# Kernel tuning notes

Hardware: AMD Instinct MI355X
Metric: run time of the kernel (lower is better)

Reference implementation:

```python
import jax, jax.numpy as jnp
import numpy as np

B, W, T, D = 8, 64, 256, 256
TI, WL, WP, G = 32, 16, 24, 64


def _ln(x, g, b):
    mu = jnp.mean(x, -1, keepdims=True)
    v = jnp.mean((x - mu) ** 2, -1, keepdims=True)
    return (x - mu) * jax.lax.rsqrt(v + 1e-5) * g + b


def _mlp2(x, w1, b1, w2, b2):
    return jax.nn.relu(x @ w1 + b1) @ w2 + b2


def setup_inputs():
    key = jax.random.key(0)
    ks = jax.random.split(key, 48)
    it = iter(range(48))
    def n(shape, s=0.02):
        return jax.random.normal(ks[next(it)], shape, jnp.float32) * s
    return {
        "task_obs": n((B, T, TI), 1.0),
        "worker_loads": n((B, W, WL), 1.0),
        "worker_profiles": n((B, W, WP), 1.0),
        "global_context": n((B, G), 1.0),
        "valid_mask": jax.random.randint(ks[next(it)], (B, T), 0, 2).astype(jnp.float32),
        "te_w1": n((TI, D)), "te_b1": jnp.zeros((D,)), "te_w2": n((D, D)), "te_b2": jnp.zeros((D,)),
        "wle_w1": n((WL, D)), "wle_b1": jnp.zeros((D,)), "wle_w2": n((D, D)), "wle_b2": jnp.zeros((D,)),
        "wpe_w1": n((WP, D)), "wpe_b1": jnp.zeros((D,)), "wpe_w2": n((D, D)), "wpe_b2": jnp.zeros((D,)),
        "ft_w": n((D, D)), "ft_b": jnp.zeros((D,)), "ft_g": jnp.ones((D,)), "ft_bt": jnp.zeros((D,)),
        "fw_w": n((2 * D, D)), "fw_b": jnp.zeros((D,)), "fw_g": jnp.ones((D,)), "fw_bt": jnp.zeros((D,)),
        "g_w1": n((G, D)), "g_b1": jnp.zeros((D,)), "g_w2": n((D, D)), "g_b2": jnp.zeros((D,)),
        "fn_g": jnp.ones((3 * D,)), "fn_b": jnp.zeros((3 * D,)),
        "actor_w": n((3 * D, 1)), "actor_b": jnp.zeros((1,)),
        "log_std": jnp.zeros((W, T)),
        "vu_w1": n((3 * D, D)), "vu_b1": jnp.zeros((D,)), "vu_w2": n((D, 1)), "vu_b2": jnp.zeros((1,)),
        "vc_w1": n((3 * D, D)), "vc_b1": jnp.zeros((D,)), "vc_w2": n((D, 1)), "vc_b2": jnp.zeros((1,)),
        "policy_id": 2,
    }


def reference(task_obs, worker_loads, worker_profiles, global_context, valid_mask, te_w1, te_b1, te_w2, te_b2, wle_w1, wle_b1, wle_w2, wle_b2, wpe_w1, wpe_b1, wpe_w2, wpe_b2, ft_w, ft_b, ft_g, ft_bt, fw_w, fw_b, fw_g, fw_bt, g_w1, g_b1, g_w2, g_b2, fn_g, fn_b, actor_w, actor_b, log_std, vu_w1, vu_b1, vu_w2, vu_b2, vc_w1, vc_b1, vc_w2, vc_b2, policy_id):
    b = task_obs.shape[0]
    # encoders (RowWiseEncoder = 2-layer MLP) + per-modality projections
    t_feat = _ln(jax.nn.relu(_mlp2(task_obs, te_w1, te_b1, te_w2, te_b2) @ ft_w + ft_b), ft_g, ft_bt)  # (B,T,D)
    wl = _mlp2(worker_loads, wle_w1, wle_b1, wle_w2, wle_b2)
    wp = _mlp2(worker_profiles, wpe_w1, wpe_b1, wpe_w2, wpe_b2)
    w_feat = _ln(jax.nn.relu(jnp.concatenate([wl, wp], -1) @ fw_w + fw_b), fw_g, fw_bt)  # (B,W,D)
    g_feat = jax.nn.relu(global_context @ g_w1 + g_b1) @ g_w2 + g_b2  # (B,D)
    # broadcast + concat fusion (B,W,T,3D), LayerNorm, actor head
    w_exp = jnp.broadcast_to(w_feat[:, :, None, :], (b, W, T, D))
    t_exp = jnp.broadcast_to(t_feat[:, None, :, :], (b, W, T, D))
    g_exp = jnp.broadcast_to(g_feat[:, None, None, :], (b, W, T, D))
    fusion = _ln(jnp.concatenate([w_exp, t_exp, g_exp], -1), fn_g, fn_b)
    mean = jax.nn.sigmoid((fusion @ actor_w)[..., 0] + actor_b[0])  # (B,W,T)
    std = jnp.broadcast_to(jnp.exp(jnp.clip(log_std, -4.0, 1.0))[None], mean.shape)
    # masked mean pooling + value heads
    mask = valid_mask[..., None]
    t_pool = (t_feat * mask).sum(1) / jnp.clip(mask.sum(1), 1.0, None)
    w_pool = w_feat.mean(1)
    vci = jnp.concatenate([t_pool, w_pool, g_feat], -1)  # (B,3D)
    v_u = _mlp2(vci, vu_w1, vu_b1, vu_w2, vu_b2)[..., 0]
    v_c = _mlp2(vci, vc_w1, vc_b1, vc_w2, vc_b2)[..., 0]
    return (mean, std, v_u, v_c)
```

## Files before the change

kernel.cpp:

```cpp
#include <hip/hip_runtime.h>
#include <math.h>

namespace {

constexpr int B_ = 8, W_ = 64, T_ = 256, D_ = 256;

typedef _Float16 h2 __attribute__((ext_vector_type(2)));
typedef _Float16 h8 __attribute__((ext_vector_type(8)));
typedef float f32x4 __attribute__((ext_vector_type(4)));
typedef __fp16 fp16v2 __attribute__((ext_vector_type(2)));

constexpr int WS_ST    = 0;
constexpr int WS_SUMT  = 2048;
constexpr int WS_SST   = 4096;
constexpr int WS_SW    = 6144;
constexpr int WS_SUMW  = 6656;
constexpr int WS_SSW   = 7168;
constexpr int WS_SG    = 7680;
constexpr int WS_SUMG  = 7688;
constexpr int WS_SSG   = 7696;
constexpr int WS_C0    = 7704;
constexpr int WS_C1    = 7705;
constexpr int WS_GFEAT = 7712;
constexpr int WS_TPP   = 9760;
constexpr int WS_WPP   = 42528;
constexpr int WS_PK    = 665120;

constexpr int FM_TE1  = 0;
constexpr int FM_TE2  = 1024;
constexpr int FM_FT   = 9216;
constexpr int FM_WLE1 = 17408;
constexpr int FM_WLE2 = 18432;
constexpr int FM_WPE1 = 26624;
constexpr int FM_WPE2 = 27648;
constexpr int FM_FW   = 35840;
constexpr int FM_END  = 52224;
constexpr int PM_G1   = 52224;
constexpr int PM_G2   = 54272;
constexpr int PM_VU1  = 62464;
constexpr int PM_VC1  = 87040;
constexpr int PK_TOTAL = 111616;

__device__ __forceinline__ float wave_sum(float v) {
#pragma unroll
  for (int m = 32; m > 0; m >>= 1) v += __shfl_xor(v, m, 64);
  return v;
}

__device__ __forceinline__ float red16(float v) {
  v += __shfl_xor(v, 1, 64);
  v += __shfl_xor(v, 2, 64);
  v += __shfl_xor(v, 4, 64);
  v += __shfl_xor(v, 8, 64);
  return v;
}

__device__ __forceinline__ unsigned pkrtz_u(float a, float b) {
  fp16v2 p = __builtin_amdgcn_cvt_pkrtz(a, b);
  return __builtin_bit_cast(unsigned, p);
}

__device__ __forceinline__ float fdot2u(unsigned x, unsigned w, float c) {
#if __has_builtin(__builtin_amdgcn_fdot2)
  return __builtin_amdgcn_fdot2(__builtin_bit_cast(h2, x),
                                __builtin_bit_cast(h2, w), c, false);
#else
  h2 a = __builtin_bit_cast(h2, x);
  h2 b = __builtin_bit_cast(h2, w);
  float r = fmaf((float)a.x, (float)b.x, c);
  return fmaf((float)a.y, (float)b.y, r);
#endif
}

template <int R, int G>
__device__ __forceinline__ void gemmp(const uint4* __restrict__ Wp,
                                      const uint4* xp, int xs, int d,
                                      float* acc) {
#pragma unroll
  for (int r = 0; r < R; ++r) acc[r] = 0.f;
#pragma unroll 4
  for (int g = 0; g < G; ++g) {
    uint4 w = Wp[g * 256 + d];
#pragma unroll
    for (int r = 0; r < R; ++r) {
      uint4 x = xp[r * xs + g];
      acc[r] = fdot2u(x.x, w.x, acc[r]);
      acc[r] = fdot2u(x.y, w.y, acc[r]);
      acc[r] = fdot2u(x.z, w.z, acc[r]);
      acc[r] = fdot2u(x.w, w.w, acc[r]);
    }
  }
}

template <int R>
__device__ __forceinline__ void shfl_pack(const float* v, unsigned* dst,
                                          int stride, int d) {
#pragma unroll
  for (int r = 0; r < R; ++r) {
    float p = __shfl_xor(v[r], 1, 64);
    unsigned pk = (d & 1) ? pkrtz_u(p, v[r]) : pkrtz_u(v[r], p);
    if (!(d & 1)) dst[r * stride + (d >> 1)] = pk;
  }
}

template <int NT, int KS, bool ACC_IN>
__device__ __forceinline__ void mfma_gemm(const uint4* __restrict__ wb,
                                          int nt0, int ks0, int l,
                                          const h8* afr, f32x4* acc) {
  uint4 bufA[KS], bufB[KS];
#pragma unroll
  for (int ks = 0; ks < KS; ++ks)
    bufA[ks] = wb[((ks0 + ks) * 16 + nt0) * 64 + l];
#pragma unroll
  for (int nt = 0; nt < NT; ++nt) {
    const uint4* cur = (nt & 1) ? bufB : bufA;
    uint4* nxt = (nt & 1) ? bufA : bufB;
    if (nt + 1 < NT) {
#pragma unroll
      for (int ks = 0; ks < KS; ++ks)
        nxt[ks] = wb[((ks0 + ks) * 16 + nt0 + nt + 1) * 64 + l];
    }
    f32x4 c;
    if (ACC_IN) c = acc[nt];
    else { c[0] = 0.f; c[1] = 0.f; c[2] = 0.f; c[3] = 0.f; }
#pragma unroll
    for (int ks = 0; ks < KS; ++ks)
      c = __builtin_amdgcn_mfma_f32_16x16x32_f16(
          afr[ks], __builtin_bit_cast(h8, cur[ks]), c, 0, 0, 0);
    acc[nt] = c;
  }
}

template <int KS>
__device__ __forceinline__ void lda(const _Float16* src, int row, int stride,
                                    int l4, h8* afr) {
#pragma unroll
  for (int ks = 0; ks < KS; ++ks)
    afr[ks] = *(const h8*)(src + row * stride + ks * 32 + 8 * l4);
}

template <int NT, bool RELU>
__device__ __forceinline__ void epi_store(const f32x4* acc,
                                          const float* __restrict__ bias,
                                          int c0, int dc0, int l15, int l4,
                                          _Float16* dst, int stride) {
#pragma unroll
  for (int nt = 0; nt < NT; ++nt) {
    float bv = bias[c0 + nt * 16 + l15];
    int dc = dc0 + nt * 16 + l15;
#pragma unroll
    for (int i = 0; i < 4; ++i) {
      float v = acc[nt][i] + bv;
      if (RELU) v = fmaxf(v, 0.f);
      dst[(l4 * 4 + i) * stride + dc] = (_Float16)v;
    }
  }
}

template <bool MASKED>
__device__ __forceinline__ void ln_block8(
    f32x4* acc, const float* __restrict__ g, const float* __restrict__ bt,
    const float* __restrict__ fn_g_seg, const float* __restrict__ aw_seg,
    const float* __restrict__ mask_base, float* stA, float* stB, int wq, int l,
    int tid, float* __restrict__ pool, float* __restrict__ Sd,
    float* __restrict__ sumd, float* __restrict__ ssd) {
  const int l15 = l & 15, l4 = l >> 4;
#pragma unroll
  for (int i = 0; i < 4; ++i) {
    float s = 0.f, ss = 0.f;
#pragma unroll
    for (int nt = 0; nt < 2; ++nt) {
      float v = acc[nt][i];
      s += v;
      ss = fmaf(v, v, ss);
    }
    s = red16(s);
    ss = red16(ss);
    if (l15 == 0) {
      int row = l4 * 4 + i;
      stA[(row * 8 + wq) * 2 + 0] = s;
      stA[(row * 8 + wq) * 2 + 1] = ss;
    }
  }
  __syncthreads();
  float gg[2], bb[2], fa[2];
#pragma unroll
  for (int nt = 0; nt < 2; ++nt) {
    int c = wq * 32 + nt * 16 + l15;
    gg[nt] = g[c];
    bb[nt] = bt[c];
    fa[nt] = fn_g_seg[c] * aw_seg[c];
  }
  float pp[2] = {0.f, 0.f};
#pragma unroll
  for (int i = 0; i < 4; ++i) {
    int row = l4 * 4 + i;
    float s = 0.f, ss = 0.f;
#pragma unroll
    for (int q = 0; q < 8; ++q) {
      s += stA[(row * 8 + q) * 2];
      ss += stA[(row * 8 + q) * 2 + 1];
    }
    float mu = s * (1.f / 256.f);
    float var = ss * (1.f / 256.f) - mu * mu;
    float inv = rsqrtf(var + 1e-5f);
    float mk = MASKED ? mask_base[row] : 1.f;
    float a1 = 0.f, a2 = 0.f, a3 = 0.f;
#pragma unroll
    for (int nt = 0; nt < 2; ++nt) {
      float v = (acc[nt][i] - mu) * inv * gg[nt] + bb[nt];
      a1 = fmaf(v, fa[nt], a1);
      a2 += v;
      a3 = fmaf(v, v, a3);
      pp[nt] = fmaf(mk, v, pp[nt]);
    }
    a1 = red16(a1);
    a2 = red16(a2);
    a3 = red16(a3);
    if (l15 == 0) {
      stB[(row * 8 + wq) * 3 + 0] = a1;
      stB[(row * 8 + wq) * 3 + 1] = a2;
      stB[(row * 8 + wq) * 3 + 2] = a3;
    }
  }
#pragma unroll
  for (int nt = 0; nt < 2; ++nt) {
    pp[nt] += __shfl_xor(pp[nt], 16, 64);
    pp[nt] += __shfl_xor(pp[nt], 32, 64);
  }
  if (l < 16) {
#pragma unroll
    for (int nt = 0; nt < 2; ++nt) pool[wq * 32 + nt * 16 + l15] = pp[nt];
  }
  __syncthreads();
  if (tid < 16) {
    int row = tid;
    float sA = 0.f, sB = 0.f, sC = 0.f;
#pragma unroll
    for (int q = 0; q < 8; ++q) {
      sA += stB[(row * 8 + q) * 3 + 0];
      sB += stB[(row * 8 + q) * 3 + 1];
      sC += stB[(row * 8 + q) * 3 + 2];
    }
    Sd[row] = sA;
    sumd[row] = sB;
    ssd[row] = sC;
  }
}

__global__ __launch_bounds__(256) void pack_kernel(
    const float* __restrict__ te_w1, const float* __restrict__ te_w2,
    const float* __restrict__ ft_w, const float* __restrict__ wle_w1,
    const float* __restrict__ wle_w2, const float* __restrict__ wpe_w1,
    const float* __restrict__ wpe_w2, const float* __restrict__ fw_w,
    const float* __restrict__ g_w1, const float* __restrict__ g_w2,
    const float* __restrict__ vu_w1, const float* __restrict__ vc_w1,
    uint4* __restrict__ dst) {
  int i = blockIdx.x * 256 + threadIdx.x;
  if (i < FM_END) {
    const float* src; int off, Ksrc;
    if      (i < FM_TE2)  { src = te_w1;  off = FM_TE1;  Ksrc = 32;  }
    else if (i < FM_FT)   { src = te_w2;  off = FM_TE2;  Ksrc = 256; }
    else if (i < FM_WLE1) { src = ft_w;   off = FM_FT;   Ksrc = 256; }
    else if (i < FM_WLE2) { src = wle_w1; off = FM_WLE1; Ksrc = 16;  }
    else if (i < FM_WPE1) { src = wle_w2; off = FM_WLE2; Ksrc = 256; }
    else if (i < FM_WPE2) { src = wpe_w1; off = FM_WPE1; Ksrc = 24;  }
    else if (i < FM_FW)   { src = wpe_w2; off = FM_WPE2; Ksrc = 256; }
    else                  { src = fw_w;   off = FM_FW;   Ksrc = 512; }
    int li = i - off;
    int l = li & 63, nt = (li >> 6) & 15, ks = li >> 10;
    int n = nt * 16 + (l & 15);
    int k0 = ks * 32 + 8 * (l >> 4);
    h8 v;
#pragma unroll
    for (int j = 0; j < 8; ++j) {
      int k = k0 + j;
      v[j] = (k < Ksrc) ? (_Float16)src[(size_t)k * 256 + n] : (_Float16)0.f;
    }
    dst[i] = __builtin_bit_cast(uint4, v);
  } else {
    const float* src; int off;
    if      (i < PM_G2)  { src = g_w1;  off = PM_G1;  }
    else if (i < PM_VU1) { src = g_w2;  off = PM_G2;  }
    else if (i < PM_VC1) { src = vu_w1; off = PM_VU1; }
    else                 { src = vc_w1; off = PM_VC1; }
    int li = i - off;
    int g = li >> 8, d = li & 255;
    const float* p = src + (size_t)g * 8 * 256 + d;
    unsigned r[4];
#pragma unroll
    for (int j = 0; j < 4; ++j) {
      h2 pk;
      pk.x = (_Float16)p[(2 * j) * 256];
      pk.y = (_Float16)p[(2 * j + 1) * 256];
      r[j] = __builtin_bit_cast(unsigned, pk);
    }
    uint4 o;
    o.x = r[0]; o.y = r[1]; o.z = r[2]; o.w = r[3];
    dst[i] = o;
  }
}

__global__ __launch_bounds__(512) void enc_kernel(
    const float* __restrict__ task_obs, const float* __restrict__ worker_loads,
    const float* __restrict__ worker_profiles,
    const float* __restrict__ global_context,
    const float* __restrict__ valid_mask, const float* __restrict__ te_b1,
    const float* __restrict__ te_b2, const float* __restrict__ wle_b1,
    const float* __restrict__ wle_b2, const float* __restrict__ wpe_b1,
    const float* __restrict__ wpe_b2, const float* __restrict__ ft_b,
    const float* __restrict__ ft_g, const float* __restrict__ ft_bt,
    const float* __restrict__ fw_b, const float* __restrict__ fw_g,
    const float* __restrict__ fw_bt, const float* __restrict__ g_b1,
    const float* __restrict__ g_b2, const float* __restrict__ fn_g,
    const float* __restrict__ fn_b, const float* __restrict__ actor_w,
    const float* __restrict__ actor_b, const uint4* __restrict__ wpk,
    float* __restrict__ ws) {
  __shared__ __align__(16) unsigned char smem[29440];
  const int tid = threadIdx.x;
  const int blk = blockIdx.x;
  const int w = tid >> 6, l = tid & 63;
  const int l15 = l & 15, l4 = l >> 4;
  const int swz = ((blk >> 3) + blk) & 7;
  const int wq = (w + swz) & 7;
  float* stA = (float*)(smem + 26880);
  float* stB = (float*)(smem + 27904);

  if (blk < 128) {
    const int rb = blk * 16;
    const int bI = rb >> 8, t0 = rb & 255;
    _Float16* hT = (_Float16*)smem;
    h8 a0;
    {
      const float* xr = task_obs + (size_t)(rb + l15) * 32 + 8 * l4;
      float4 xa = *(const float4*)xr;
      float4 xb = *(const float4*)(xr + 4);
      a0[0] = (_Float16)xa.x; a0[1] = (_Float16)xa.y;
      a0[2] = (_Float16)xa.z; a0[3] = (_Float16)xa.w;
      a0[4] = (_Float16)xb.x; a0[5] = (_Float16)xb.y;
      a0[6] = (_Float16)xb.z; a0[7] = (_Float16)xb.w;
    }
    f32x4 acc[2];
    mfma_gemm<2, 1, false>(wpk + FM_TE1, 2 * wq, 0, l, &a0, acc);
    epi_store<2, true>(acc, te_b1, wq * 32, wq * 32, l15, l4, hT, 264);
    __syncthreads();
    h8 afr[8];
    lda<8>(hT, l15, 264, l4, afr);
    __syncthreads();
    mfma_gemm<2, 8, false>(wpk + FM_TE2, 2 * wq, 0, l, afr, acc);
    epi_store<2, false>(acc, te_b2, wq * 32, wq * 32, l15, l4, hT, 264);
    __syncthreads();
    lda<8>(hT, l15, 264, l4, afr);
    mfma_gemm<2, 8, false>(wpk + FM_FT, 2 * wq, 0, l, afr, acc);
#pragma unroll
    for (int nt = 0; nt < 2; ++nt) {
      float bv = ft_b[wq * 32 + nt * 16 + l15];
#pragma unroll
      for (int i = 0; i < 4; ++i) acc[nt][i] = fmaxf(acc[nt][i] + bv, 0.f);
    }
    ln_block8<true>(acc, ft_g, ft_bt, fn_g + 256, actor_w + 256,
                    valid_mask + bI * 256 + t0, stA, stB, wq, l, tid,
                    ws + WS_TPP + blk * 256, ws + WS_ST + rb, ws + WS_SUMT + rb,
                    ws + WS_SST + rb);
  } else if (blk < 160) {
    const int wbl = blk - 128;
    const int rbw = wbl * 16;
    _Float16* XW = (_Float16*)smem;
    _Float16* h1 = (_Float16*)(smem + 1536);
    _Float16* ct = (_Float16*)(smem + 9984);
    if (tid < 256) {
      int r = tid >> 4, k = tid & 15;
      XW[r * 48 + k] = (_Float16)worker_loads[(size_t)(rbw + r) * 16 + k];
      XW[r * 48 + 16 + k] = (_Float16)0.f;
    }
    __syncthreads();
    h8 ax = *(const h8*)(XW + l15 * 48 + 8 * l4);
    f32x4 acc[2];
    mfma_gemm<2, 1, false>(wpk + FM_WLE1, 2 * wq, 0, l, &ax, acc);
    epi_store<2, true>(acc, wle_b1, wq * 32, wq * 32, l15, l4, h1, 264);
    __syncthreads();
    h8 afr[8];
    lda<8>(h1, l15, 264, l4, afr);
    for (int e = tid; e < 384; e += 512) {
      int r = e / 24, k = e - r * 24;
      XW[r * 48 + k] = (_Float16)worker_profiles[(size_t)(rbw + r) * 24 + k];
    }
    if (tid < 128) {
      int r = tid >> 3, k = 24 + (tid & 7);
      XW[r * 48 + k] = (_Float16)0.f;
    }
    __syncthreads();
    mfma_gemm<2, 8, false>(wpk + FM_WLE2, 2 * wq, 0, l, afr, acc);
    epi_store<2, false>(acc, wle_b2, wq * 32, wq * 32, l15, l4, ct, 528);
    ax = *(const h8*)(XW + l15 * 48 + 8 * l4);
    mfma_gemm<2, 1, false>(wpk + FM_WPE1, 2 * wq, 0, l, &ax, acc);
    epi_store<2, true>(acc, wpe_b1, wq * 32, wq * 32, l15, l4, h1, 264);
    __syncthreads();
    lda<8>(h1, l15, 264, l4, afr);
    mfma_gemm<2, 8, false>(wpk + FM_WPE2, 2 * wq, 0, l, afr, acc);
    epi_store<2, false>(acc, wpe_b2, wq * 32, 256 + wq * 32, l15, l4, ct, 528);
    __syncthreads();
    h8 af2[16];
    lda<16>(ct, l15, 528, l4, af2);
    mfma_gemm<2, 8, false>(wpk + FM_FW, 2 * wq, 0, l, af2, acc);
    mfma_gemm<2, 8, true>(wpk + FM_FW, 2 * wq, 8, l, af2 + 8, acc);
#pragma unroll
    for (int nt = 0; nt < 2; ++nt) {
      float bv = fw_b[wq * 32 + nt * 16 + l15];
#pragma unroll
      for (int i = 0; i < 4; ++i) acc[nt][i] = fmaxf(acc[nt][i] + bv, 0.f);
    }
    ln_block8<false>(acc, fw_g, fw_bt, fn_g, actor_w, nullptr, stA, stB, wq, l,
                     tid, ws + WS_WPP + wbl * 256, ws + WS_SW + rbw,
                     ws + WS_SUMW + rbw, ws + WS_SSW + rbw);
  } else {
    float* smf = (float*)smem;
    unsigned* smp = (unsigned*)(smem + 8256);
    const int d = tid & 255;
    if (tid < 256)
      smp[tid] = pkrtz_u(global_context[2 * tid], global_context[2 * tid + 1]);
    __syncthreads();
    float acc[8], v[8];
    if (tid < 256) {
      gemmp<8, 8>(wpk + PM_G1, (const uint4*)smp, 8, d, acc);
      float b = g_b1[d];
#pragma unroll
      for (int r = 0; r < 8; ++r) v[r] = fmaxf(acc[r] + b, 0.f);
      shfl_pack<8>(v, smp + 256, 128, d);
    }
    __syncthreads();
    if (tid < 256) {
      gemmp<8, 32>(wpk + PM_G2, (const uint4*)(smp + 256), 32, d, acc);
      float b = g_b2[d];
#pragma unroll
      for (int r = 0; r < 8; ++r) {
        float x = acc[r] + b;
        ws[WS_GFEAT + r * D_ + d] = x;
        smf[r * D_ + d] = x;
      }
      float c0 = 0.f, c1 = 0.f;
      for (int i = tid; i < 768; i += 256) {
        float aw = actor_w[i];
        c0 = fmaf(fn_b[i], aw, c0);
        c1 = fmaf(fn_g[i], aw, c1);
      }
      c0 = wave_sum(c0);
      c1 = wave_sum(c1);
      const int wv = tid >> 6, lane = tid & 63;
      if (lane == 0) {
        smf[2048 + wv] = c0;
        smf[2052 + wv] = c1;
      }
    }
    __syncthreads();
    if (tid < 256) {
      const int wv = tid >> 6, lane = tid & 63;
      for (int r = wv; r < 8; r += 4) {
        float a1 = 0.f, a2 = 0.f, a3 = 0.f;
        for (int j = lane; j < D_; j += 64) {
          float x = smf[r * D_ + j];
          a1 = fmaf(x, fn_g[512 + j] * actor_w[512 + j], a1);
          a2 += x;
          a3 = fmaf(x, x, a3);
        }
        a1 = wave_sum(a1);
        a2 = wave_sum(a2);
        a3 = wave_sum(a3);
        if (lane == 0) {
          ws[WS_SG + r] = a1;
          ws[WS_SUMG + r] = a2;
          ws[WS_SSG + r] = a3;
        }
      }
      if (tid == 0) {
        ws[WS_C0] = smf[2048] + smf[2049] + smf[2050] + smf[2051] + actor_b[0];
        ws[WS_C1] = smf[2052] + smf[2053] + smf[2054] + smf[2055];
      }
    }
  }
}

__global__ __launch_bounds__(256) void head_kernel(
    const float* __restrict__ valid_mask, const float* __restrict__ log_std,
    const float* __restrict__ vu_b1, const float* __restrict__ vu_b2,
    const float* __restrict__ vc_b1, const float* __restrict__ vc_b2,
    const float* __restrict__ vu_w2, const float* __restrict__ vc_w2,
    const uint4* __restrict__ wpk, const float* __restrict__ ws,
    float* __restrict__ out) {
  const int tid = threadIdx.x;
  const int blk = blockIdx.x;
  if (blk < 16) {
    const int head = blk >> 3;
    const int b = blk & 7;
    __shared__ float lm[256];
    __shared__ float red[8];
    __shared__ __align__(16) unsigned vcip[384];
    lm[tid] = valid_mask[b * T_ + tid];
    __syncthreads();
    float m = wave_sum(lm[tid]);
    if ((tid & 63) == 0) red[tid >> 6] = m;
    __syncthreads();
    const float mdiv = 1.f / fmaxf(red[0] + red[1] + red[2] + red[3], 1.f);
    float vv[3];
    {
      float acc = 0.f;
#pragma unroll
      for (int c = 0; c < 16; ++c)
        acc += ws[WS_TPP + (b * 16 + c) * 256 + tid];
      vv[0] = acc * mdiv;
      acc = 0.f;
#pragma unroll
      for (int c = 0; c < 4; ++c) acc += ws[WS_WPP + (b * 4 + c) * 256 + tid];
      vv[1] = acc * (1.f / 64.f);
      vv[2] = ws[WS_GFEAT + b * D_ + tid];
    }
    shfl_pack<3>(vv, vcip, 128, tid);
    __syncthreads();
    const uint4* w1p = wpk + (head ? PM_VC1 : PM_VU1);
    const float* b1 = head ? vc_b1 : vu_b1;
    const float* w2 = head ? vc_w2 : vu_w2;
    const float* b2 = head ? vc_b2 : vu_b2;
    float h = 0.f;
    const uint4* xq = (const uint4*)vcip;
    int g = (blk & 7) * 12;
#pragma unroll 8
    for (int it = 0; it < 96; ++it) {
      uint4 w = w1p[g * 256 + tid];
      uint4 x = xq[g];
      h = fdot2u(x.x, w.x, h);
      h = fdot2u(x.y, w.y, h);
      h = fdot2u(x.z, w.z, h);
      h = fdot2u(x.w, w.w, h);
      ++g;
      if (g == 96) g = 0;
    }
    h = fmaxf(h + b1[tid], 0.f);
    float c = wave_sum(h * w2[tid]);
    __syncthreads();
    if ((tid & 63) == 0) red[tid >> 6] = c;
    __syncthreads();
    if (tid == 0)
      out[2 * B_ * W_ * T_ + head * B_ + b] =
          red[0] + red[1] + red[2] + red[3] + b2[0];
  } else {
    const int base = (blk - 16) * 512 + tid * 2;
    const float C0 = ws[WS_C0];
    const float C1 = ws[WS_C1];
#pragma unroll
    for (int e = 0; e < 2; ++e) {
      const int idx = base + e;
      const int b = idx >> 14;
      const int w = (idx >> 8) & 63;
      const int t = idx & 255;
      float S = ws[WS_SW + b * W_ + w] + ws[WS_ST + b * T_ + t] + ws[WS_SG + b];
      float sum =
          ws[WS_SUMW + b * W_ + w] + ws[WS_SUMT + b * T_ + t] + ws[WS_SUMG + b];
      float ssq =
          ws[WS_SSW + b * W_ + w] + ws[WS_SST + b * T_ + t] + ws[WS_SSG + b];
      float mu = sum * (1.f / 768.f);
      float var = ssq * (1.f / 768.f) - mu * mu;
      float inv = rsqrtf(var + 1e-5f);
      float logit = inv * (S - mu * C1) + C0;
      out[idx] = 1.f / (1.f + expf(-logit));
      float ls = log_std[w * T_ + t];
      out[B_ * W_ * T_ + idx] = expf(fminf(fmaxf(ls, -4.f), 1.f));
    }
  }
}

}

extern "C" void kernel_launch(void* const* d_in, const int* in_sizes, int n_in,
                              void* d_out, int out_size, void* d_ws,
                              size_t ws_size, hipStream_t stream) {
  (void)in_sizes; (void)n_in; (void)out_size; (void)ws_size;
  const float* task_obs        = (const float*)d_in[0];
  const float* worker_loads    = (const float*)d_in[1];
  const float* worker_profiles = (const float*)d_in[2];
  const float* global_context  = (const float*)d_in[3];
  const float* valid_mask      = (const float*)d_in[4];
  const float* te_w1  = (const float*)d_in[5];
  const float* te_b1  = (const float*)d_in[6];
  const float* te_w2  = (const float*)d_in[7];
  const float* te_b2  = (const float*)d_in[8];
  const float* wle_w1 = (const float*)d_in[9];
  const float* wle_b1 = (const float*)d_in[10];
  const float* wle_w2 = (const float*)d_in[11];
  const float* wle_b2 = (const float*)d_in[12];
  const float* wpe_w1 = (const float*)d_in[13];
  const float* wpe_b1 = (const float*)d_in[14];
  const float* wpe_w2 = (const float*)d_in[15];
  const float* wpe_b2 = (const float*)d_in[16];
  const float* ft_w   = (const float*)d_in[17];
  const float* ft_b   = (const float*)d_in[18];
  const float* ft_g   = (const float*)d_in[19];
  const float* ft_bt  = (const float*)d_in[20];
  const float* fw_w   = (const float*)d_in[21];
  const float* fw_b   = (const float*)d_in[22];
  const float* fw_g   = (const float*)d_in[23];
  const float* fw_bt  = (const float*)d_in[24];
  const float* g_w1   = (const float*)d_in[25];
  const float* g_b1   = (const float*)d_in[26];
  const float* g_w2   = (const float*)d_in[27];
  const float* g_b2   = (const float*)d_in[28];
  const float* fn_g   = (const float*)d_in[29];
  const float* fn_b   = (const float*)d_in[30];
  const float* actor_w = (const float*)d_in[31];
  const float* actor_b = (const float*)d_in[32];
  const float* log_std = (const float*)d_in[33];
  const float* vu_w1  = (const float*)d_in[34];
  const float* vu_b1  = (const float*)d_in[35];
  const float* vu_w2  = (const float*)d_in[36];
  const float* vu_b2  = (const float*)d_in[37];
  const float* vc_w1  = (const float*)d_in[38];
  const float* vc_b1  = (const float*)d_in[39];
  const float* vc_w2  = (const float*)d_in[40];
  const float* vc_b2  = (const float*)d_in[41];
  float* ws = (float*)d_ws;
  uint4* wpk = (uint4*)(ws + WS_PK);
  float* out = (float*)d_out;

  hipLaunchKernelGGL(pack_kernel, dim3(PK_TOTAL / 256), dim3(256), 0, stream,
                     te_w1, te_w2, ft_w, wle_w1, wle_w2, wpe_w1, wpe_w2, fw_w,
                     g_w1, g_w2, vu_w1, vc_w1, wpk);
  hipLaunchKernelGGL(enc_kernel, dim3(161), dim3(512), 0, stream, task_obs,
                     worker_loads, worker_profiles, global_context, valid_mask,
                     te_b1, te_b2, wle_b1, wle_b2, wpe_b1, wpe_b2, ft_b, ft_g,
                     ft_bt, fw_b, fw_g, fw_bt, g_b1, g_b2, fn_g, fn_b, actor_w,
                     actor_b, (const uint4*)wpk, ws);
  hipLaunchKernelGGL(head_kernel, dim3(272), dim3(256), 0, stream, valid_mask,
                     log_std, vu_b1, vu_b2, vc_b1, vc_b2, vu_w2, vc_w2,
                     (const uint4*)wpk, (const float*)ws, out);
}
```

Measured before the change: 34.62 us.

## Prefetch next-stage MFMA weight fragments into registers ahead of dependent GEMMs

Weight B-fragments for each subsequent GEMM stage are now loaded into registers before the preceding stage's epilogue and barriers, instead of being fetched right before each GEMM. Global-memory latency for the weights can then overlap with shared-memory staging, syncs and earlier MFMA work in both the task and worker encoder branches. The cost is more live vector registers (up to 48 uint4 fragments held at once), which may lower occupancy or cause spills.

```diff
diff --git a/kernel.cpp b/kernel.cpp
--- a/kernel.cpp
+++ b/kernel.cpp
@@ -103,32 +103,40 @@
   }
 }
 
+template <int NT, int KS>
+__device__ __forceinline__ void load_bfrags(const uint4* __restrict__ wb,
+                                            int nt0, int ks0, int l,
+                                            uint4* pf) {
+#pragma unroll
+  for (int nt = 0; nt < NT; ++nt)
+#pragma unroll
+    for (int ks = 0; ks < KS; ++ks)
+      pf[nt * KS + ks] = wb[((ks0 + ks) * 16 + nt0 + nt) * 64 + l];
+}
+
+template <int NT, int KS, bool ACC_IN>
+__device__ __forceinline__ void mfma_from(const uint4* pf, const h8* afr,
+                                          f32x4* acc) {
+#pragma unroll
+  for (int nt = 0; nt < NT; ++nt) {
+    f32x4 c;
+    if (ACC_IN) c = acc[nt];
+    else { c[0] = 0.f; c[1] = 0.f; c[2] = 0.f; c[3] = 0.f; }
+#pragma unroll
+    for (int ks = 0; ks < KS; ++ks)
+      c = __builtin_amdgcn_mfma_f32_16x16x32_f16(
+          afr[ks], __builtin_bit_cast(h8, pf[nt * KS + ks]), c, 0, 0, 0);
+    acc[nt] = c;
+  }
+}
+
 template <int NT, int KS, bool ACC_IN>
 __device__ __forceinline__ void mfma_gemm(const uint4* __restrict__ wb,
                                           int nt0, int ks0, int l,
                                           const h8* afr, f32x4* acc) {
-  uint4 bufA[KS], bufB[KS];
-#pragma unroll
-  for (int ks = 0; ks < KS; ++ks)
-    bufA[ks] = wb[((ks0 + ks) * 16 + nt0) * 64 + l];
-#pragma unroll
-  for (int nt = 0; nt < NT; ++nt) {
-    const uint4* cur = (nt & 1) ? bufB : bufA;
-    uint4* nxt = (nt & 1) ? bufA : bufB;
-    if (nt + 1 < NT) {
-#pragma unroll
-      for (int ks = 0; ks < KS; ++ks)
-        nxt[ks] = wb[((ks0 + ks) * 16 + nt0 + nt + 1) * 64 + l];
-    }
-    f32x4 c;
-    if (ACC_IN) c = acc[nt];
-    else { c[0] = 0.f; c[1] = 0.f; c[2] = 0.f; c[3] = 0.f; }
-#pragma unroll
-    for (int ks = 0; ks < KS; ++ks)
-      c = __builtin_amdgcn_mfma_f32_16x16x32_f16(
-          afr[ks], __builtin_bit_cast(h8, cur[ks]), c, 0, 0, 0);
-    acc[nt] = c;
-  }
+  uint4 pf[NT * KS];
+  load_bfrags<NT, KS>(wb, nt0, ks0, l, pf);
+  mfma_from<NT, KS, ACC_IN>(pf, afr, acc);
 }
 
 template <int KS>
@@ -330,6 +338,8 @@
     const int rb = blk * 16;
     const int bI = rb >> 8, t0 = rb & 255;
     _Float16* hT = (_Float16*)smem;
+    uint4 pfA[16];
+    load_bfrags<2, 8>(wpk + FM_TE2, 2 * wq, 0, l, pfA);
     h8 a0;
     {
       const float* xr = task_obs + (size_t)(rb + l15) * 32 + 8 * l4;
@@ -347,11 +357,13 @@
     h8 afr[8];
     lda<8>(hT, l15, 264, l4, afr);
     __syncthreads();
-    mfma_gemm<2, 8, false>(wpk + FM_TE2, 2 * wq, 0, l, afr, acc);
+    uint4 pfB[16];
+    load_bfrags<2, 8>(wpk + FM_FT, 2 * wq, 0, l, pfB);
+    mfma_from<2, 8, false>(pfA, afr, acc);
     epi_store<2, false>(acc, te_b2, wq * 32, wq * 32, l15, l4, hT, 264);
     __syncthreads();
     lda<8>(hT, l15, 264, l4, afr);
-    mfma_gemm<2, 8, false>(wpk + FM_FT, 2 * wq, 0, l, afr, acc);
+    mfma_from<2, 8, false>(pfB, afr, acc);
 #pragma unroll
     for (int nt = 0; nt < 2; ++nt) {
       float bv = ft_b[wq * 32 + nt * 16 + l15];
@@ -368,6 +380,8 @@
     _Float16* XW = (_Float16*)smem;
     _Float16* h1 = (_Float16*)(smem + 1536);
     _Float16* ct = (_Float16*)(smem + 9984);
+    uint4 pfA[16];
+    load_bfrags<2, 8>(wpk + FM_WLE2, 2 * wq, 0, l, pfA);
     if (tid < 256) {
       int r = tid >> 4, k = tid & 15;
       XW[r * 48 + k] = (_Float16)worker_loads[(size_t)(rbw + r) * 16 + k];
@@ -381,6 +395,8 @@
     __syncthreads();
     h8 afr[8];
     lda<8>(h1, l15, 264, l4, afr);
+    uint4 pfB[16];
+    load_bfrags<2, 8>(wpk + FM_WPE2, 2 * wq, 0, l, pfB);
     for (int e = tid; e < 384; e += 512) {
       int r = e / 24, k = e - r * 24;
       XW[r * 48 + k] = (_Float16)worker_profiles[(size_t)(rbw + r) * 24 + k];
@@ -390,19 +406,21 @@
       XW[r * 48 + k] = (_Float16)0.f;
     }
     __syncthreads();
-    mfma_gemm<2, 8, false>(wpk + FM_WLE2, 2 * wq, 0, l, afr, acc);
+    mfma_from<2, 8, false>(pfA, afr, acc);
     epi_store<2, false>(acc, wle_b2, wq * 32, wq * 32, l15, l4, ct, 528);
     ax = *(const h8*)(XW + l15 * 48 + 8 * l4);
     mfma_gemm<2, 1, false>(wpk + FM_WPE1, 2 * wq, 0, l, &ax, acc);
     epi_store<2, true>(acc, wpe_b1, wq * 32, wq * 32, l15, l4, h1, 264);
     __syncthreads();
     lda<8>(h1, l15, 264, l4, afr);
-    mfma_gemm<2, 8, false>(wpk + FM_WPE2, 2 * wq, 0, l, afr, acc);
+    uint4 pfC[16];
+    load_bfrags<2, 8>(wpk + FM_FW, 2 * wq, 0, l, pfC);
+    mfma_from<2, 8, false>(pfB, afr, acc);
     epi_store<2, false>(acc, wpe_b2, wq * 32, 256 + wq * 32, l15, l4, ct, 528);
     __syncthreads();
     h8 af2[16];
     lda<16>(ct, l15, 528, l4, af2);
-    mfma_gemm<2, 8, false>(wpk + FM_FW, 2 * wq, 0, l, af2, acc);
+    mfma_from<2, 8, false>(pfC, af2, acc);
     mfma_gemm<2, 8, true>(wpk + FM_FW, 2 * wq, 8, l, af2 + 8, acc);
 #pragma unroll
     for (int nt = 0; nt < 2; ++nt) {
```

New measurement: 30.26 us. 1.14x faster.
